# Performance work log

Measured on AMD Instinct MI355X. Metric: run time of the kernel, lower is better.

The kernel has to match this reference:

```python
import jax, jax.numpy as jnp
import numpy as np

B, T, E, H = 1024, 200, 128, 128
N_ITEMS, N_CATS = 100000, 1000
LN_EPS = 1e-5


def _prelu(x, a):
    return jnp.where(x >= 0, x, a * x)


def _layernorm(x, g, b):
    m = x.mean(-1, keepdims=True)
    v = ((x - m) ** 2).mean(-1, keepdims=True)
    return (x - m) / jnp.sqrt(v + LN_EPS) * g + b


def setup_inputs() -> dict:
    key = jax.random.key(0)
    it = iter(jax.random.split(key, 64))
    nx = lambda: next(it)
    def lin(out_d, in_d):
        s = 1.0 / np.sqrt(in_d)
        return jax.random.uniform(nx(), (out_d, in_d), jnp.float32, -s, s)
    inp = {}
    inp['behavior_ids'] = jax.random.randint(nx(), (B, T), 0, N_ITEMS)
    inp['candidate_id'] = jax.random.randint(nx(), (B,), 0, N_ITEMS)
    inp['candidate_cat'] = jax.random.randint(nx(), (B,), 0, N_CATS)
    inp['dense_features'] = jax.random.normal(nx(), (B, 5), jnp.float32)
    inp['item_emb'] = (jax.random.normal(nx(), (N_ITEMS, E), jnp.float32) * 0.01).at[0].set(0.0)
    inp['cat_emb'] = (jax.random.normal(nx(), (N_CATS, E // 2), jnp.float32) * 0.01).at[0].set(0.0)
    # nn.GRU params (gate order r,z,n)
    inp['gru_wih'] = lin(3 * H, E)
    inp['gru_whh'] = lin(3 * H, H)
    inp['gru_bih'] = jnp.zeros((3 * H,), jnp.float32)
    inp['gru_bhh'] = jnp.zeros((3 * H,), jnp.float32)
    # auxiliary_net: Linear(H,E) -> ReLU -> Linear(E,1)
    inp['aux_w1'] = lin(E, H); inp['aux_b1'] = jnp.zeros((E,), jnp.float32)
    inp['aux_w2'] = lin(1, E); inp['aux_b2'] = jnp.zeros((1,), jnp.float32)
    # attention_mlp: Linear(3H,64) -> PReLU -> Linear(64,1)
    inp['att_w1'] = lin(64, 3 * H); inp['att_b1'] = jnp.zeros((64,), jnp.float32)
    inp['att_a'] = jnp.array(0.25, jnp.float32)
    inp['att_w2'] = lin(1, 64); inp['att_b2'] = jnp.zeros((1,), jnp.float32)
    # AUGRU gates: Linear(2H, H) each
    inp['wz'] = lin(H, 2 * H); inp['bz'] = jnp.zeros((H,), jnp.float32)
    inp['wr'] = lin(H, 2 * H); inp['br'] = jnp.zeros((H,), jnp.float32)
    inp['wh'] = lin(H, 2 * H); inp['bh'] = jnp.zeros((H,), jnp.float32)
    # dense_proj Linear(5,32)
    inp['dp_w'] = lin(32, 5); inp['dp_b'] = jnp.zeros((32,), jnp.float32)
    # MLP: 352 -> 256 -> 128 -> 64, each Linear + LayerNorm + PReLU
    dims = [H + E + E // 2 + 32, 256, 128, 64]
    for i in range(3):
        inp[f'm_w{i+1}'] = lin(dims[i + 1], dims[i])
        inp[f'm_b{i+1}'] = jnp.zeros((dims[i + 1],), jnp.float32)
        inp[f'ln_g{i+1}'] = jnp.ones((dims[i + 1],), jnp.float32)
        inp[f'ln_b{i+1}'] = jnp.zeros((dims[i + 1],), jnp.float32)
        inp[f'pa{i+1}'] = jnp.array(0.25, jnp.float32)
    # 3 task heads Linear(64,1), stacked
    inp['heads_w'] = lin(3, 64); inp['heads_b'] = jnp.zeros((3,), jnp.float32)
    return inp


def _forward_core(behavior_ids, candidate_id, candidate_cat, dense_features,
                  item_emb, cat_emb, gru_wih, gru_whh, gru_bih, gru_bhh,
                  aux_w1, aux_b1, aux_w2, aux_b2,
                  att_w1, att_b1, att_a, att_w2, att_b2,
                  wz, bz, wr, br, wh, bh, dp_w, dp_b,
                  m_w1, m_b1, ln_g1, ln_b1, pa1,
                  m_w2, m_b2, ln_g2, ln_b2, pa2,
                  m_w3, m_b3, ln_g3, ln_b3, pa3,
                  heads_w, heads_b):
    beh = item_emb[behavior_ids]            # [B,T,E]
    cand = item_emb[candidate_id]           # [B,E]
    catv = cat_emb[candidate_cat]           # [B,E//2]
    Bsz = beh.shape[0]
    Hd = gru_whh.shape[1]
    h0 = jnp.zeros((Bsz, Hd), beh.dtype)
    # --- interest extractor GRU (cuDNN GRU math, gate order r,z,n) ---
    xp = jnp.einsum('bte,ge->btg', beh, gru_wih) + gru_bih  # [B,T,3H]
    def gru_step(h, x):
        hp = h @ gru_whh.T + gru_bhh
        xr, xz, xn = jnp.split(x, 3, -1)
        hr, hz, hn = jnp.split(hp, 3, -1)
        r = jax.nn.sigmoid(xr + hr)
        z = jax.nn.sigmoid(xz + hz)
        n = jnp.tanh(xn + r * hn)
        hnew = (1 - z) * n + z * h
        return hnew, hnew
    _, hs = jax.lax.scan(gru_step, h0, jnp.swapaxes(xp, 0, 1))
    hs = jnp.swapaxes(hs, 0, 1)             # [B,T,H]
    # --- auxiliary logits ---
    aux = jax.nn.relu(hs[:, :-1] @ aux_w1.T + aux_b1) @ aux_w2.T + aux_b2  # [B,T-1,1]
    # --- attention (embed_dim == hidden_size so cand_proj == candidate_emb) ---
    ce = cand[:, None, :]
    att_in = jnp.concatenate([hs, jnp.broadcast_to(ce, hs.shape), hs * ce], -1)  # [B,T,3H]
    scores = (_prelu(att_in @ att_w1.T + att_b1, att_a) @ att_w2.T + att_b2)[..., 0]
    att = jax.nn.softmax(scores, axis=-1)   # [B,T]
    # --- AUGRU: attention-modulated update gate ---
    def augru_step(h, xs):
        x, a = xs                           # x: [B,H], a: [B]
        comb = jnp.concatenate([x, h], -1)
        z = jax.nn.sigmoid(comb @ wz.T + bz)
        r = jax.nn.sigmoid(comb @ wr.T + br)
        comb_r = jnp.concatenate([x, r * h], -1)
        ht = jnp.tanh(comb_r @ wh.T + bh)
        zp = a[:, None] * z
        return (1 - zp) * h + zp * ht, None
    hT, _ = jax.lax.scan(augru_step, h0, (jnp.swapaxes(hs, 0, 1), att.T))
    # --- fusion MLP (dropout is identity in eval) ---
    dense_out = dense_features @ dp_w.T + dp_b
    x = jnp.concatenate([hT, cand, catv, dense_out], -1)  # [B,352]
    for (w, b, g, be, a) in ((m_w1, m_b1, ln_g1, ln_b1, pa1),
                             (m_w2, m_b2, ln_g2, ln_b2, pa2),
                             (m_w3, m_b3, ln_g3, ln_b3, pa3)):
        x = _prelu(_layernorm(x @ w.T + b, g, be), a)
    preds = jax.nn.sigmoid(x @ heads_w.T + heads_b)  # [B,3] == 3 heads of [B,1]
    return preds, aux


def reference(behavior_ids, candidate_id, candidate_cat, dense_features,
              item_emb, cat_emb, gru_wih, gru_whh, gru_bih, gru_bhh,
              aux_w1, aux_b1, aux_w2, aux_b2,
              att_w1, att_b1, att_a, att_w2, att_b2,
              wz, bz, wr, br, wh, bh, dp_w, dp_b,
              m_w1, m_b1, ln_g1, ln_b1, pa1,
              m_w2, m_b2, ln_g2, ln_b2, pa2,
              m_w3, m_b3, ln_g3, ln_b3, pa3,
              heads_w, heads_b):
    return _forward_core(behavior_ids, candidate_id, candidate_cat, dense_features,
                         item_emb, cat_emb, gru_wih, gru_whh, gru_bih, gru_bhh,
                         aux_w1, aux_b1, aux_w2, aux_b2,
                         att_w1, att_b1, att_a, att_w2, att_b2,
                         wz, bz, wr, br, wh, bh, dp_w, dp_b,
                         m_w1, m_b1, ln_g1, ln_b1, pa1,
                         m_w2, m_b2, ln_g2, ln_b2, pa2,
                         m_w3, m_b3, ln_g3, ln_b3, pa3,
                         heads_w, heads_b)
```

## Files before the change

### kernel.cpp

```cpp
#include <hip/hip_runtime.h>


typedef __bf16 bf16;
typedef float f32x4 __attribute__((ext_vector_type(4)));
typedef __bf16 bf16x8 __attribute__((ext_vector_type(8)));
typedef __bf16 bf16x4 __attribute__((ext_vector_type(4)));

#define MFMA16(a, b, c) __builtin_amdgcn_mfma_f32_16x16x32_bf16((a), (b), (c), 0, 0, 0)

#define BATCH 1024
#define SEQT 200
#define F32_ONE 0x3F800000u

__device__ __forceinline__ float sigm(float x) {
  return __builtin_amdgcn_rcpf(1.0f + __expf(-x));
}
__device__ __forceinline__ float tanh_fast(float x) {
  float ax = fabsf(x);
  float t = 1.0f - 2.0f * __builtin_amdgcn_rcpf(__expf(2.0f * ax) + 1.0f);
  return copysignf(t, x);
}

__device__ __forceinline__ void bar_lgkm() {
  asm volatile("s_waitcnt lgkmcnt(0)\n\ts_barrier" ::: "memory");
// ... 3 lines not shown
  __builtin_amdgcn_global_load_lds((__attribute__((address_space(1))) void*)g,
                                   (__attribute__((address_space(3))) void*)l,
                                   16, 0, 0);
}

template <typename DT> __device__ __forceinline__ float ldf(const DT* p, long i);
template <> __device__ __forceinline__ float ldf<bf16>(const bf16* p, long i) { return (float)p[i]; }
template <> __device__ __forceinline__ float ldf<float>(const float* p, long i) { return p[i]; }

template <typename DT> __device__ __forceinline__ bf16x8 ld8(const DT* p, long i);
template <> __device__ __forceinline__ bf16x8 ld8<bf16>(const bf16* p, long i) {
  return *(const bf16x8*)(p + i);
}
template <> __device__ __forceinline__ bf16x8 ld8<float>(const float* p, long i) {
  f32x4 a = *(const f32x4*)(p + i);
  f32x4 b = *(const f32x4*)(p + i + 4);
  bf16x8 r;
  r[0] = (bf16)a[0]; r[1] = (bf16)a[1]; r[2] = (bf16)a[2]; r[3] = (bf16)a[3];
  r[4] = (bf16)b[0]; r[5] = (bf16)b[1]; r[6] = (bf16)b[2]; r[7] = (bf16)b[3];
  return r;
}

template <typename DT>
__device__ __forceinline__ void prep_body(
    const int* __restrict__ cid, const int* __restrict__ ccat,
    const DT* __restrict__ dense, const DT* __restrict__ item_emb,
    const DT* __restrict__ cat_emb, const DT* __restrict__ dp_w,
    const DT* __restrict__ dp_b, bf16* __restrict__ candbuf, bf16* __restrict__ xf) {
  const int b = blockIdx.x;
  const int t = threadIdx.x;
  bf16 v = (bf16)ldf(item_emb, (long)cid[b] * 128 + t);
  candbuf[b * 128 + t] = v;
  xf[(long)b * 352 + 128 + t] = v;
  if (t < 64) xf[(long)b * 352 + 256 + t] = (bf16)ldf(cat_emb, (long)ccat[b] * 64 + t);
  if (t < 32) {
    float s = ldf(dp_b, t);
    for (int k = 0; k < 5; k++) s += ldf(dense, b * 5 + k) * ldf(dp_w, t * 5 + k);
    xf[(long)b * 352 + 320 + t] = (bf16)s;
  }
}
__global__ __launch_bounds__(128) void k_prep(
    const unsigned* __restrict__ disc, const int* cid, const int* ccat,
    const void* dense, const void* item_emb, const void* cat_emb,
    const void* dp_w, const void* dp_b, bf16* candbuf, bf16* xf) {
  if (*disc == F32_ONE)
    prep_body<float>(cid, ccat, (const float*)dense, (const float*)item_emb,
                     (const float*)cat_emb, (const float*)dp_w, (const float*)dp_b, candbuf, xf);
  else
    prep_body<bf16>(cid, ccat, (const bf16*)dense, (const bf16*)item_emb,
                    (const bf16*)cat_emb, (const bf16*)dp_w, (const bf16*)dp_b, candbuf, xf);
}

template <typename DT>
__device__ __forceinline__ void gru3_body(
    const int* __restrict__ ids, const DT* __restrict__ item_emb,
    const DT* __restrict__ wih, const DT* __restrict__ whh,
    const DT* __restrict__ bih, const DT* __restrict__ bhh, bf16* __restrict__ hs,
    bf16 (*hA)[16][136], bf16 (*xb)[4][16][136], char* raw) {
  const int b0 = blockIdx.x * 16;
  const int tid = threadIdx.x;
  const int w = tid >> 6, lane = tid & 63, l15 = lane & 15, quad = lane >> 4;
  const int nc = w * 16 + l15;

  for (int i = tid; i < 2 * 16 * 136; i += 512) ((bf16*)hA)[i] = (bf16)0.0f;

  bf16x8 wir[4], wiz[4], win_[4], whr[4], whz[4], whn[4];
#pragma unroll
  for (int k = 0; k < 4; k++) {
    const long off = k * 32 + quad * 8;
    wir[k] = ld8(wih, (long)nc * 128 + off);
    wiz[k] = ld8(wih, (long)(128 + nc) * 128 + off);
    win_[k] = ld8(wih, (long)(256 + nc) * 128 + off);
    whr[k] = ld8(whh, (long)nc * 128 + off);
    whz[k] = ld8(whh, (long)(128 + nc) * 128 + off);
    whn[k] = ld8(whh, (long)(256 + nc) * 128 + off);
  }
  const float br_s = ldf(bih, nc) + ldf(bhh, nc);
  const float bz_s = ldf(bih, 128 + nc) + ldf(bhh, 128 + nc);
  const float bxn_s = ldf(bih, 256 + nc);
  const float bhn_s = ldf(bhh, 256 + nc);

  const int idrow = (sizeof(DT) == 4) ? (tid >> 5) : ((tid >> 4) & 15);
  const int* idbase = ids + (long)(b0 + idrow) * SEQT;

  auto DMA = [&](const int4 id4) {
    if constexpr (sizeof(DT) == 4) {
#pragma unroll
      for (int j = 0; j < 4; j++)
        dma16((const char*)(item_emb + (long)((&id4.x)[j]) * 128) + (tid & 31) * 16,
              raw + (j * 512 + tid) * 16);
    } else {
#pragma unroll
      for (int j = 0; j < 2; j++) {
        const int slot = j * 2 + (tid >> 8);
        dma16((const char*)(item_emb + (long)((&id4.x)[slot]) * 128) + (tid & 15) * 16,
              raw + (j * 512 + tid) * 16);
      }
    }
  };
  auto CONV = [&](int buf) {
    if constexpr (sizeof(DT) == 4) {
      const float* rf = (const float*)raw;
#pragma unroll
      for (int h = 0; h < 4; h++) {
        const int e = h * 2048 + tid * 4;
        f32x4 a = *(const f32x4*)(rf + e);
        const int slot = e >> 11, row = (e >> 7) & 15, col = e & 127;
        bf16x4 o;
        o[0] = (bf16)a[0]; o[1] = (bf16)a[1]; o[2] = (bf16)a[2]; o[3] = (bf16)a[3];
        *(bf16x4*)&xb[buf][slot][row][col] = o;
      }
    } else {
      const bf16* rh = (const bf16*)raw;
#pragma unroll
      for (int h = 0; h < 2; h++) {
        const int e = h * 4096 + tid * 8;
        const int slot = e >> 11, row = (e >> 7) & 15, col = e & 127;
        *(bf16x8*)&xb[buf][slot][row][col] = *(const bf16x8*)(rh + e);
      }
    }
  };

  const int srow = tid >> 5, sch = (tid & 31) * 4;
  bf16* hsb = hs + ((long)(b0 + srow) * SEQT) * 128 + sch;

  float hreg[4] = {0.f, 0.f, 0.f, 0.f};
  const f32x4 z4 = {0.f, 0.f, 0.f, 0.f};

  int4 idv = *(const int4*)(idbase);
  DMA(idv);
  idv = *(const int4*)(idbase + 4);
  asm volatile("s_waitcnt vmcnt(1)" ::: "memory");
  __builtin_amdgcn_sched_barrier(0);
  __builtin_amdgcn_s_barrier();
  CONV(0);
  asm volatile("s_waitcnt lgkmcnt(0)" ::: "memory");
  __builtin_amdgcn_sched_barrier(0);
  __builtin_amdgcn_s_barrier();
  DMA(idv);
  idv = *(const int4*)(idbase + 8);

#define GRU_STEP(P, S)                                                         \
  {                                                                            \
    const int tt = t0 + (S);                                                   \
    bf16x8 af[4], xaf[4];                                                      \
    _Pragma("unroll") for (int k = 0; k < 4; k++) {                            \
      af[k] = *(const bf16x8*)&hA[P][l15][k * 32 + quad * 8];                  \
      xaf[k] = *(const bf16x8*)&xb[buf][S][l15][k * 32 + quad * 8];            \
    }                                                                          \
    { const int slot = tt ? tt - 1 : 0;                                        \
      bf16x4 hv = *(const bf16x4*)&hA[P][srow][sch];                           \
      *(bf16x4*)(hsb + (long)slot * 128) = hv; }                               \
    f32x4 ar = z4, az = z4, axn = z4, ahn = z4;                                \
    _Pragma("unroll") for (int k = 0; k < 4; k++) {                            \
      ar = MFMA16(xaf[k], wir[k], ar);                                         \
      az = MFMA16(xaf[k], wiz[k], az);                                         \
      axn = MFMA16(xaf[k], win_[k], axn);                                      \
    }                                                                          \
    _Pragma("unroll") for (int k = 0; k < 4; k++) {                            \
      ar = MFMA16(af[k], whr[k], ar);                                          \
      az = MFMA16(af[k], whz[k], az);                                          \
      ahn = MFMA16(af[k], whn[k], ahn);                                        \
    }                                                                          \
    _Pragma("unroll") for (int r = 0; r < 4; r++) {                            \
      float r_ = sigm(ar[r] + br_s);                                           \
      float z_ = sigm(az[r] + bz_s);                                           \
      float n_ = tanh_fast(axn[r] + bxn_s + r_ * (ahn[r] + bhn_s));            \
      float hnew = (1.0f - z_) * n_ + z_ * hreg[r];                            \
      hreg[r] = hnew;                                                          \
      hA[(P) ^ 1][quad * 4 + r][nc] = (bf16)hnew;                              \
    }                                                                          \
    bar_lgkm();                                                                \
  }

  for (int c = 0; c < 50; c++) {
    const int t0 = c * 4;
    const int buf = c & 1;
    GRU_STEP(0, 0) GRU_STEP(1, 1) GRU_STEP(0, 2) GRU_STEP(1, 3)
    if (c < 49) {
      asm volatile("s_waitcnt vmcnt(4)" ::: "memory");
      __builtin_amdgcn_sched_barrier(0);
      __builtin_amdgcn_s_barrier();
      CONV((c + 1) & 1);
      asm volatile("s_waitcnt lgkmcnt(0)" ::: "memory");
      __builtin_amdgcn_sched_barrier(0);
      __builtin_amdgcn_s_barrier();
      if (c < 48) {
        DMA(idv);
        int nid = (c + 3) * 4; if (nid > 196) nid = 196;
        idv = *(const int4*)(idbase + nid);
      }
    }
  }
#undef GRU_STEP
  { bf16x4 hv = *(const bf16x4*)&hA[0][srow][sch];
    *(bf16x4*)(hsb + (long)(SEQT - 1) * 128) = hv; }
}
__global__ __launch_bounds__(512, 1) void k_gru3(
    const unsigned* __restrict__ disc, const int* ids, const void* item_emb,
    const void* wih, const void* whh, const void* bih, const void* bhh, bf16* hs) {
  __shared__ __align__(16) bf16 hA[2][16][136];
  __shared__ __align__(16) bf16 xb[2][4][16][136];
  __shared__ __align__(16) char raw[32768];
  if (*disc == F32_ONE)
    gru3_body<float>(ids, (const float*)item_emb, (const float*)wih, (const float*)whh,
                     (const float*)bih, (const float*)bhh, hs, hA, xb, raw);
  else
    gru3_body<bf16>(ids, (const bf16*)item_emb, (const bf16*)wih, (const bf16*)whh,
                    (const bf16*)bih, (const bf16*)bhh, hs, hA, xb, raw);
}

template <typename DT>
__device__ __forceinline__ void attaux_body(
    const bf16* __restrict__ hs, const int* __restrict__ cid,
    const DT* __restrict__ item_emb,
    const DT* __restrict__ aw1, const DT* __restrict__ ab1,
    const DT* __restrict__ aw2, const DT* __restrict__ ab2,
    const DT* __restrict__ tw1, const DT* __restrict__ tb1, const DT* __restrict__ ta,
    const DT* __restrict__ tw2, const DT* __restrict__ tb2,
    float* __restrict__ sc, float* __restrict__ outaux,
    bf16 (*As)[64][128], float (*scPt)[64], float (*scPa)[64]) {
  const int t0 = blockIdx.x * 64;
  const int b0 = blockIdx.y * 16;
  const int tid = threadIdx.x, w = tid >> 6, lane = tid & 63, l15 = lane & 15, quad = lane >> 4;

  const int tn = w * 16 + l15;
  bf16x8 wth[4], wtc[4], wthc[4], wa0[4], wa1[4];
#pragma unroll
  for (int k = 0; k < 4; k++) {
    const long off = k * 32 + quad * 8;
    wth[k]  = ld8(tw1, (long)tn * 384 + off);
    wtc[k]  = ld8(tw1, (long)tn * 384 + 128 + off);
    wthc[k] = ld8(tw1, (long)tn * 384 + 256 + off);
    wa0[k]  = ld8(aw1, (long)((2 * w) * 16 + l15) * 128 + off);
    wa1[k]  = ld8(aw1, (long)((2 * w + 1) * 16 + l15) * 128 + off);
  }
  const float tb1c = ldf(tb1, tn), tw2c = ldf(tw2, tn);
  const float ab1c0 = ldf(ab1, (2 * w) * 16 + l15), aw2c0 = ldf(aw2, (2 * w) * 16 + l15);
  const float ab1c1 = ldf(ab1, (2 * w + 1) * 16 + l15), aw2c1 = ldf(aw2, (2 * w + 1) * 16 + l15);
  const float aP = ldf(ta, 0), tb2s = ldf(tb2, 0), ab2s = ldf(ab2, 0);

  auto DMA = [&](int b, int buf) {
#pragma unroll
    for (int c = 0; c < 4; c++) {
      const int idx = c * 256 + tid;
      const int row = idx >> 4, p = idx & 15;
      int t = t0 + row; if (t > SEQT - 1) t = SEQT - 1;
      const bf16* src = hs + ((long)b * SEQT + t) * 128 + ((p ^ (row & 7)) * 8);
      dma16(src, (char*)(&As[buf][0][0]) + idx * 16);
    }
  };
  auto CANDLD = [&](int b, bf16x8* cf) {
#pragma unroll
    for (int k = 0; k < 4; k++)
      cf[k] = ld8(item_emb, (long)cid[b] * 128 + k * 32 + quad * 8);
  };

  const f32x4 z4 = {0.f, 0.f, 0.f, 0.f};
  bf16x8 candA[4], candB[4];
  DMA(b0, 0);
  CANDLD(b0, candA);
  asm volatile("s_waitcnt vmcnt(0)" ::: "memory");
// ... 54 lines not shown
      int tt2 = tid - 64, t = t0 + tt2;                                        \
      if (t < SEQT - 1) {                                                      \
        float s = scPa[0][tt2] + scPa[1][tt2] + scPa[2][tt2] + scPa[3][tt2];   \
        outaux[(long)b * 199 + t] = s + ab2s;                                  \
      }                                                                        \
    }                                                                          \
    asm volatile("s_waitcnt vmcnt(0) lgkmcnt(0)" ::: "memory");                \
    __builtin_amdgcn_sched_barrier(0);                                         \
    __builtin_amdgcn_s_barrier();                                              \
  }

  for (int bi = 0; bi < 16; bi += 2) {
    AA_STEP(bi, candA, candB)
    AA_STEP(bi + 1, candB, candA)
  }
#undef AA_STEP
}
__global__ __launch_bounds__(256, 1) void k_attaux(
    const unsigned* __restrict__ disc, const bf16* hs, const int* cid,
    const void* item_emb,
    const void* aw1, const void* ab1, const void* aw2, const void* ab2,
    const void* tw1, const void* tb1, const void* ta, const void* tw2, const void* tb2,
    float* sc, float* outaux) {
  __shared__ __align__(16) bf16 As[2][64][128];
  __shared__ __align__(16) float scPt[4][64];
  __shared__ __align__(16) float scPa[4][64];
  if (*disc == F32_ONE)
    attaux_body<float>(hs, cid, (const float*)item_emb,
                       (const float*)aw1, (const float*)ab1, (const float*)aw2, (const float*)ab2,
                       (const float*)tw1, (const float*)tb1, (const float*)ta,
                       (const float*)tw2, (const float*)tb2, sc, outaux, As, scPt, scPa);
  else
    attaux_body<bf16>(hs, cid, (const bf16*)item_emb,
                      (const bf16*)aw1, (const bf16*)ab1, (const bf16*)aw2, (const bf16*)ab2,
                      (const bf16*)tw1, (const bf16*)tb1, (const bf16*)ta,
                      (const bf16*)tw2, (const bf16*)tb2, sc, outaux, As, scPt, scPa);
}

__global__ __launch_bounds__(256) void k_softmax(float* __restrict__ sc) {
  const int b = blockIdx.x, tid = threadIdx.x;
  __shared__ float red[256];
  float v = (tid < SEQT) ? sc[(long)b * SEQT + tid] : -1e30f;
  red[tid] = v; __syncthreads();
  for (int s = 128; s > 0; s >>= 1) { if (tid < s) red[tid] = fmaxf(red[tid], red[tid + s]); __syncthreads(); }
  float mx = red[0]; __syncthreads();
  float e = (tid < SEQT) ? __expf(v - mx) : 0.f;
  red[tid] = e; __syncthreads();
  for (int s = 128; s > 0; s >>= 1) { if (tid < s) red[tid] += red[tid + s]; __syncthreads(); }
  float inv = 1.0f / red[0];
  if (tid < SEQT) sc[(long)b * SEQT + tid] = e * inv;
}

template <typename DT>
__device__ __forceinline__ void augru3_body(
    const bf16* __restrict__ hsrc, const float* __restrict__ att,
    const DT* __restrict__ wz, const DT* __restrict__ wr, const DT* __restrict__ wh,
    const DT* __restrict__ bzv, const DT* __restrict__ brv, const DT* __restrict__ bhv,
    bf16* __restrict__ xf_out,
    bf16 (*hA)[16][136], bf16 (*rhA)[136], float (*attL)[201],
    bf16 (*xb)[4][16][136], char* raw) {
  const int b0 = blockIdx.x * 16;
  const int tid = threadIdx.x;
  const int w = tid >> 6, lane = tid & 63, l15 = lane & 15, quad = lane >> 4;
  const int nc = w * 16 + l15;

  for (int i = tid; i < 2 * 16 * 136; i += 512) ((bf16*)hA)[i] = (bf16)0.0f;
  for (int i = tid; i < 16 * SEQT; i += 512) {
    int r = i / SEQT, c = i - r * SEQT;
    attL[r][c] = att[(long)(b0 + r) * SEQT + c];
  }

  bf16x8 wzx[4], wzh[4], wrx[4], wrh[4], whx[4], whh_[4];
#pragma unroll
  for (int k = 0; k < 4; k++) {
    const long off = k * 32 + quad * 8;
    wzx[k] = ld8(wz, (long)nc * 256 + off);
    wzh[k] = ld8(wz, (long)nc * 256 + 128 + off);
    wrx[k] = ld8(wr, (long)nc * 256 + off);
    wrh[k] = ld8(wr, (long)nc * 256 + 128 + off);
    whx[k] = ld8(wh, (long)nc * 256 + off);
    whh_[k] = ld8(wh, (long)nc * 256 + 128 + off);
  }
  const float bz_s = ldf(bzv, nc);
  const float br_s = ldf(brv, nc);
  const float bh_s = ldf(bhv, nc);

  auto DMA = [&](int t0) {
#pragma unroll
    for (int j = 0; j < 2; j++) {
      const int slot = j * 2 + (tid >> 8);
      const int row = (tid >> 4) & 15;
      const bf16* src = hsrc + ((long)(b0 + row) * SEQT + t0 + slot) * 128 + (tid & 15) * 8;
      dma16(src, raw + (j * 512 + tid) * 16);
    }
  };
  auto CONV = [&](int buf) {
    const bf16* rh = (const bf16*)raw;
#pragma unroll
    for (int h = 0; h < 2; h++) {
      const int e = h * 4096 + tid * 8;
      const int slot = e >> 11, row = (e >> 7) & 15, col = e & 127;
      *(bf16x8*)&xb[buf][slot][row][col] = *(const bf16x8*)(rh + e);
    }
  };

  float hreg[4] = {0.f, 0.f, 0.f, 0.f};
  const f32x4 z4 = {0.f, 0.f, 0.f, 0.f};

  DMA(0);
  asm volatile("s_waitcnt vmcnt(0)" ::: "memory");
  __builtin_amdgcn_sched_barrier(0);
  __builtin_amdgcn_s_barrier();
  CONV(0);
  asm volatile("s_waitcnt lgkmcnt(0)" ::: "memory");
  __builtin_amdgcn_sched_barrier(0);
  __builtin_amdgcn_s_barrier();
  DMA(4);

#define AUGRU_STEP(P, S)                                                       \
  {                                                                            \
    const int tt = t0 + (S);                                                   \
    bf16x8 af[4], xaf[4];                                                      \
    _Pragma("unroll") for (int k = 0; k < 4; k++) {                            \
      af[k] = *(const bf16x8*)&hA[P][l15][k * 32 + quad * 8];                  \
      xaf[k] = *(const bf16x8*)&xb[buf][S][l15][k * 32 + quad * 8];            \
    }                                                                          \
    f32x4 az = z4, ar = z4, axh = z4;                                          \
    _Pragma("unroll") for (int k = 0; k < 4; k++) {                            \
      az = MFMA16(xaf[k], wzx[k], az);                                         \
      ar = MFMA16(xaf[k], wrx[k], ar);                                         \
      axh = MFMA16(xaf[k], whx[k], axh);                                       \
    }                                                                          \
    _Pragma("unroll") for (int k = 0; k < 4; k++) {                            \
      az = MFMA16(af[k], wzh[k], az);                                          \
      ar = MFMA16(af[k], wrh[k], ar);                                          \
    }                                                                          \
    float zp[4];                                                               \
    _Pragma("unroll") for (int r = 0; r < 4; r++) {                            \
      float a_ = attL[quad * 4 + r][tt];                                       \
      float z_ = sigm(az[r] + bz_s);                                           \
      float r_ = sigm(ar[r] + br_s);                                           \
      zp[r] = a_ * z_;                                                         \
      rhA[quad * 4 + r][nc] = (bf16)(r_ * hreg[r]);                            \
    }                                                                          \
    bar_lgkm();                                                                \
    bf16x8 rf[4];                                                              \
    _Pragma("unroll") for (int k = 0; k < 4; k++)                              \
      rf[k] = *(const bf16x8*)&rhA[l15][k * 32 + quad * 8];                    \
    f32x4 ahh = axh;                                                           \
    _Pragma("unroll") for (int k = 0; k < 4; k++)                              \
      ahh = MFMA16(rf[k], whh_[k], ahh);                                       \
    _Pragma("unroll") for (int r = 0; r < 4; r++) {                            \
      float ht = tanh_fast(ahh[r] + bh_s);                                     \
      float hnew = (1.f - zp[r]) * hreg[r] + zp[r] * ht;                       \
      hreg[r] = hnew;                                                          \
      hA[(P) ^ 1][quad * 4 + r][nc] = (bf16)hnew;                              \
    }                                                                          \
    bar_lgkm();                                                                \
  }

  for (int c = 0; c < 50; c++) {
    const int t0 = c * 4;
    const int buf = c & 1;
    AUGRU_STEP(0, 0) AUGRU_STEP(1, 1) AUGRU_STEP(0, 2) AUGRU_STEP(1, 3)
    if (c < 49) {
      asm volatile("s_waitcnt vmcnt(0)" ::: "memory");
      __builtin_amdgcn_sched_barrier(0);
      __builtin_amdgcn_s_barrier();
      CONV((c + 1) & 1);
      asm volatile("s_waitcnt lgkmcnt(0)" ::: "memory");
      __builtin_amdgcn_sched_barrier(0);
      __builtin_amdgcn_s_barrier();
      if (c < 48) DMA((c + 2) * 4);
    }
  }
#undef AUGRU_STEP
#pragma unroll
  for (int r = 0; r < 4; r++)
    xf_out[(long)(b0 + quad * 4 + r) * 352 + nc] = (bf16)hreg[r];
}
__global__ __launch_bounds__(512, 1) void k_augru3(
    const unsigned* __restrict__ disc, const bf16* hsrc, const float* att,
    const void* wz, const void* wr, const void* wh,
    const void* bzv, const void* brv, const void* bhv, bf16* xf_out) {
  __shared__ __align__(16) bf16 hA[2][16][136];
  __shared__ __align__(16) bf16 rhA[16][136];
  __shared__ __align__(16) float attL[16][201];
  __shared__ __align__(16) bf16 xb[2][4][16][136];
  __shared__ __align__(16) char raw[16384];
  if (*disc == F32_ONE)
    augru3_body<float>(hsrc, att, (const float*)wz, (const float*)wr, (const float*)wh,
                       (const float*)bzv, (const float*)brv, (const float*)bhv, xf_out,
                       hA, rhA, attL, xb, raw);
  else
    augru3_body<bf16>(hsrc, att, (const bf16*)wz, (const bf16*)wr, (const bf16*)wh,
                      (const bf16*)bzv, (const bf16*)brv, (const bf16*)bhv, xf_out,
                      hA, rhA, attL, xb, raw);
}

template <typename DT>
__device__ __forceinline__ void mlp_body(
    const bf16* __restrict__ xf,
    const DT* __restrict__ w1, const DT* __restrict__ b1, const DT* __restrict__ g1, const DT* __restrict__ be1, const DT* __restrict__ pa1,
    const DT* __restrict__ w2, const DT* __restrict__ b2, const DT* __restrict__ g2, const DT* __restrict__ be2, const DT* __restrict__ pa2,
    const DT* __restrict__ w3, const DT* __restrict__ b3, const DT* __restrict__ g3, const DT* __restrict__ be3, const DT* __restrict__ pa3,
    const DT* __restrict__ hw, const DT* __restrict__ hb, float* __restrict__ preds,
    float (*xs)[352], float (*ys)[256]) {
  const int tid = threadIdx.x, w = tid >> 6, lane = tid & 63;
  const int b = blockIdx.x * 4 + w;
  for (int i = lane; i < 352; i += 64) xs[w][i] = (float)xf[(long)b * 352 + i];
  __syncthreads();
  float acc1[4];
#pragma unroll
  for (int oi = 0; oi < 4; oi++) {
    int o = lane + 64 * oi;
    float s = ldf(b1, o);
    for (int k = 0; k < 352; k += 8) {
      bf16x8 wv = ld8(w1, (long)o * 352 + k);
#pragma unroll
      for (int j = 0; j < 8; j++) s += xs[w][k + j] * (float)wv[j];
    }
    acc1[oi] = s;
  }
  float sm = acc1[0] + acc1[1] + acc1[2] + acc1[3];
#pragma unroll
  for (int m = 1; m < 64; m <<= 1) sm += __shfl_xor(sm, m, 64);
  float mean = sm * (1.0f / 256.0f);
  float vs = 0.f;
#pragma unroll
  for (int oi = 0; oi < 4; oi++) { float d = acc1[oi] - mean; vs += d * d; }
#pragma unroll
  for (int m = 1; m < 64; m <<= 1) vs += __shfl_xor(vs, m, 64);
  float rstd = rsqrtf(vs * (1.0f / 256.0f) + 1e-5f);
  float a1 = ldf(pa1, 0);
#pragma unroll
  for (int oi = 0; oi < 4; oi++) {
    int o = lane + 64 * oi;
    float y = (acc1[oi] - mean) * rstd * ldf(g1, o) + ldf(be1, o);
    ys[w][o] = (y >= 0.f) ? y : a1 * y;
  }
  __syncthreads();
  float acc2[2];
#pragma unroll
  for (int oi = 0; oi < 2; oi++) {
    int o = lane + 64 * oi;
    float s = ldf(b2, o);
    for (int k = 0; k < 256; k += 8) {
      bf16x8 wv = ld8(w2, (long)o * 256 + k);
#pragma unroll
      for (int j = 0; j < 8; j++) s += ys[w][k + j] * (float)wv[j];
// ... 77 lines not shown
  const void* item_emb = d_in[4];
  const void* cat_emb = d_in[5];
  const void* gru_wih = d_in[6];
  const void* gru_whh = d_in[7];
  const void* gru_bih = d_in[8];
  const void* gru_bhh = d_in[9];
  const void* aux_w1 = d_in[10];
  const void* aux_b1 = d_in[11];
  const void* aux_w2 = d_in[12];
  const void* aux_b2 = d_in[13];
  const void* att_w1 = d_in[14];
  const void* att_b1 = d_in[15];
  const void* att_a = d_in[16];
  const void* att_w2 = d_in[17];
  const void* att_b2 = d_in[18];
  const void* wz = d_in[19];
  const void* bz = d_in[20];
  const void* wr = d_in[21];
  const void* br = d_in[22];
  const void* wh = d_in[23];
  const void* bh = d_in[24];
  const void* dp_w = d_in[25];
  const void* dp_b = d_in[26];
  const void* m_w1 = d_in[27];
  const void* m_b1 = d_in[28];
  const void* ln_g1 = d_in[29];
  const void* ln_b1 = d_in[30];
  const void* pa1 = d_in[31];
  const void* m_w2 = d_in[32];
  const void* m_b2 = d_in[33];
  const void* ln_g2 = d_in[34];
  const void* ln_b2 = d_in[35];
  const void* pa2 = d_in[36];
  const void* m_w3 = d_in[37];
  const void* m_b3 = d_in[38];
  const void* ln_g3 = d_in[39];
  const void* ln_b3 = d_in[40];
  const void* pa3 = d_in[41];
  const void* heads_w = d_in[42];
  const void* heads_b = d_in[43];
  (void)in_sizes; (void)n_in; (void)out_size; (void)ws_size;

  const unsigned* disc = (const unsigned*)ln_g1;

  char* ws = (char*)d_ws;
  bf16* HS = (bf16*)(ws);
  float* SC = (float*)(ws + 52428800L);
  bf16* CAND = (bf16*)(ws + 53248000L);
  bf16* XF = (bf16*)(ws + 53510144L);
  float* OUT = (float*)d_out;

  k_prep<<<BATCH, 128, 0, stream>>>(disc, candidate_id, candidate_cat, dense, item_emb,
                                    cat_emb, dp_w, dp_b, CAND, XF);
  k_gru3<<<64, 512, 0, stream>>>(disc, behavior_ids, item_emb, gru_wih, gru_whh,
                                 gru_bih, gru_bhh, HS);
  k_attaux<<<dim3(4, 64), 256, 0, stream>>>(disc, HS, candidate_id, item_emb,
                                            aux_w1, aux_b1, aux_w2, aux_b2,
                                            att_w1, att_b1, att_a, att_w2, att_b2,
                                            SC, OUT + 3072);
  k_softmax<<<BATCH, 256, 0, stream>>>(SC);
  k_augru3<<<64, 512, 0, stream>>>(disc, HS, SC, wz, wr, wh, bz, br, bh, XF);
  k_mlp<<<256, 256, 0, stream>>>(disc, XF,
      m_w1, m_b1, ln_g1, ln_b1, pa1,
      m_w2, m_b2, ln_g2, ln_b2, pa2,
      m_w3, m_b3, ln_g3, ln_b3, pa3,
      heads_w, heads_b, OUT);
}
```

Before: 727.2 us.

## Process two independent 16-row batch groups per block in GRU and AUGRU kernels

Each GRU and AUGRU block now carries two independent 16-sequence groups through the recurrence, interleaving their MFMA chains and sharing the register-resident weight fragments, so the grid drops from 64 to 32 blocks. The aim is to hide MFMA and transcendental latency on the serial recurrence by giving each wave two independent dependency chains per barrier. The cost is half as many blocks on a GPU with many CUs, plus higher register and LDS use that could cause spills.

```diff
diff --git a/kernel.cpp b/kernel.cpp
--- a/kernel.cpp
+++ b/kernel.cpp
@@ -79,17 +79,17 @@
 }
 
 template <typename DT>
-__device__ __forceinline__ void gru3_body(
+__device__ __forceinline__ void gru4_body(
     const int* __restrict__ ids, const DT* __restrict__ item_emb,
     const DT* __restrict__ wih, const DT* __restrict__ whh,
     const DT* __restrict__ bih, const DT* __restrict__ bhh, bf16* __restrict__ hs,
-    bf16 (*hA)[16][136], bf16 (*xb)[4][16][136], char* raw) {
-  const int b0 = blockIdx.x * 16;
+    bf16 (*hA)[2][16][136], bf16 (*xb)[2][4][16][136], char* raw) {
+  const int b0 = blockIdx.x * 32;
   const int tid = threadIdx.x;
   const int w = tid >> 6, lane = tid & 63, l15 = lane & 15, quad = lane >> 4;
   const int nc = w * 16 + l15;
 
-  for (int i = tid; i < 2 * 16 * 136; i += 512) ((bf16*)hA)[i] = (bf16)0.0f;
+  for (int i = tid; i < 2 * 2 * 16 * 136; i += 512) ((bf16*)hA)[i] = (bf16)0.0f;
 
   bf16x8 wir[4], wiz[4], win_[4], whr[4], whz[4], whn[4];
 #pragma unroll
@@ -108,94 +108,121 @@
   const float bhn_s = ldf(bhh, 256 + nc);
 
   const int idrow = (sizeof(DT) == 4) ? (tid >> 5) : ((tid >> 4) & 15);
-  const int* idbase = ids + (long)(b0 + idrow) * SEQT;
-
-  auto DMA = [&](const int4 id4) {
+  const int* idbaseA = ids + (long)(b0 + idrow) * SEQT;
+  const int* idbaseB = ids + (long)(b0 + 16 + idrow) * SEQT;
+
+  auto DMA = [&](int p, const int4 id4) {
+    char* rp = raw + p * 32768;
     if constexpr (sizeof(DT) == 4) {
 #pragma unroll
       for (int j = 0; j < 4; j++)
         dma16((const char*)(item_emb + (long)((&id4.x)[j]) * 128) + (tid & 31) * 16,
-              raw + (j * 512 + tid) * 16);
+              rp + (j * 512 + tid) * 16);
     } else {
 #pragma unroll
       for (int j = 0; j < 2; j++) {
         const int slot = j * 2 + (tid >> 8);
         dma16((const char*)(item_emb + (long)((&id4.x)[slot]) * 128) + (tid & 15) * 16,
-              raw + (j * 512 + tid) * 16);
+              rp + (j * 512 + tid) * 16);
       }
     }
   };
   auto CONV = [&](int buf) {
-    if constexpr (sizeof(DT) == 4) {
-      const float* rf = (const float*)raw;
-#pragma unroll
-      for (int h = 0; h < 4; h++) {
-        const int e = h * 2048 + tid * 4;
-        f32x4 a = *(const f32x4*)(rf + e);
-        const int slot = e >> 11, row = (e >> 7) & 15, col = e & 127;
-        bf16x4 o;
-        o[0] = (bf16)a[0]; o[1] = (bf16)a[1]; o[2] = (bf16)a[2]; o[3] = (bf16)a[3];
-        *(bf16x4*)&xb[buf][slot][row][col] = o;
+#pragma unroll
+    for (int p = 0; p < 2; p++) {
+      if constexpr (sizeof(DT) == 4) {
+        const float* rf = (const float*)(raw + p * 32768);
+#pragma unroll
+        for (int h = 0; h < 4; h++) {
+          const int e = h * 2048 + tid * 4;
+          f32x4 a = *(const f32x4*)(rf + e);
+          const int slot = e >> 11, row = (e >> 7) & 15, col = e & 127;
+          bf16x4 o;
+          o[0] = (bf16)a[0]; o[1] = (bf16)a[1]; o[2] = (bf16)a[2]; o[3] = (bf16)a[3];
+          *(bf16x4*)&xb[p][buf][slot][row][col] = o;
+        }
+      } else {
+        const bf16* rh = (const bf16*)(raw + p * 32768);
+#pragma unroll
+        for (int h = 0; h < 2; h++) {
+          const int e = h * 4096 + tid * 8;
+          const int slot = e >> 11, row = (e >> 7) & 15, col = e & 127;
+          *(bf16x8*)&xb[p][buf][slot][row][col] = *(const bf16x8*)(rh + e);
+        }
       }
-    } else {
-      const bf16* rh = (const bf16*)raw;
-#pragma unroll
-      for (int h = 0; h < 2; h++) {
-        const int e = h * 4096 + tid * 8;
-        const int slot = e >> 11, row = (e >> 7) & 15, col = e & 127;
-        *(bf16x8*)&xb[buf][slot][row][col] = *(const bf16x8*)(rh + e);
-      }
     }
   };
 
   const int srow = tid >> 5, sch = (tid & 31) * 4;
-  bf16* hsb = hs + ((long)(b0 + srow) * SEQT) * 128 + sch;
-
-  float hreg[4] = {0.f, 0.f, 0.f, 0.f};
+  bf16* hsbA = hs + ((long)(b0 + srow) * SEQT) * 128 + sch;
+  bf16* hsbB = hs + ((long)(b0 + 16 + srow) * SEQT) * 128 + sch;
+
+  float hregA[4] = {0.f, 0.f, 0.f, 0.f};
+  float hregB[4] = {0.f, 0.f, 0.f, 0.f};
   const f32x4 z4 = {0.f, 0.f, 0.f, 0.f};
 
-  int4 idv = *(const int4*)(idbase);
-  DMA(idv);
-  idv = *(const int4*)(idbase + 4);
-  asm volatile("s_waitcnt vmcnt(1)" ::: "memory");
+  int4 idvA = *(const int4*)(idbaseA);
+  int4 idvB = *(const int4*)(idbaseB);
+  DMA(0, idvA); DMA(1, idvB);
+  idvA = *(const int4*)(idbaseA + 4);
+  idvB = *(const int4*)(idbaseB + 4);
+  asm volatile("s_waitcnt vmcnt(2)" ::: "memory");
   __builtin_amdgcn_sched_barrier(0);
   __builtin_amdgcn_s_barrier();
   CONV(0);
   asm volatile("s_waitcnt lgkmcnt(0)" ::: "memory");
   __builtin_amdgcn_sched_barrier(0);
   __builtin_amdgcn_s_barrier();
-  DMA(idv);
-  idv = *(const int4*)(idbase + 8);
-
-#define GRU_STEP(P, S)                                                         \
+  DMA(0, idvA); DMA(1, idvB);
+  idvA = *(const int4*)(idbaseA + 8);
+  idvB = *(const int4*)(idbaseB + 8);
+
+#define GRU_STEP2(P, S)                                                        \
   {                                                                            \
     const int tt = t0 + (S);                                                   \
-    bf16x8 af[4], xaf[4];                                                      \
+    bf16x8 afA[4], xafA[4], afB[4], xafB[4];                                   \
     _Pragma("unroll") for (int k = 0; k < 4; k++) {                            \
-      af[k] = *(const bf16x8*)&hA[P][l15][k * 32 + quad * 8];                  \
-      xaf[k] = *(const bf16x8*)&xb[buf][S][l15][k * 32 + quad * 8];            \
+      afA[k] = *(const bf16x8*)&hA[0][P][l15][k * 32 + quad * 8];              \
+      xafA[k] = *(const bf16x8*)&xb[0][buf][S][l15][k * 32 + quad * 8];        \
+      afB[k] = *(const bf16x8*)&hA[1][P][l15][k * 32 + quad * 8];              \
+      xafB[k] = *(const bf16x8*)&xb[1][buf][S][l15][k * 32 + quad * 8];        \
     }                                                                          \
     { const int slot = tt ? tt - 1 : 0;                                        \
-      bf16x4 hv = *(const bf16x4*)&hA[P][srow][sch];                           \
-      *(bf16x4*)(hsb + (long)slot * 128) = hv; }                               \
-    f32x4 ar = z4, az = z4, axn = z4, ahn = z4;                                \
+      bf16x4 hvA = *(const bf16x4*)&hA[0][P][srow][sch];                       \
+      bf16x4 hvB = *(const bf16x4*)&hA[1][P][srow][sch];                       \
+      *(bf16x4*)(hsbA + (long)slot * 128) = hvA;                               \
+      *(bf16x4*)(hsbB + (long)slot * 128) = hvB; }                             \
+    f32x4 arA = z4, azA = z4, axnA = z4, ahnA = z4;                            \
+    f32x4 arB = z4, azB = z4, axnB = z4, ahnB = z4;                            \
     _Pragma("unroll") for (int k = 0; k < 4; k++) {                            \
-      ar = MFMA16(xaf[k], wir[k], ar);                                         \
-      az = MFMA16(xaf[k], wiz[k], az);                                         \
-      axn = MFMA16(xaf[k], win_[k], axn);                                      \
+      arA = MFMA16(xafA[k], wir[k], arA);                                      \
+      azA = MFMA16(xafA[k], wiz[k], azA);                                      \
+      axnA = MFMA16(xafA[k], win_[k], axnA);                                   \
+      arB = MFMA16(xafB[k], wir[k], arB);                                      \
+      azB = MFMA16(xafB[k], wiz[k], azB);                                      \
+      axnB = MFMA16(xafB[k], win_[k], axnB);                                   \
     }                                                                          \
     _Pragma("unroll") for (int k = 0; k < 4; k++) {                            \
-      ar = MFMA16(af[k], whr[k], ar);                                          \
-      az = MFMA16(af[k], whz[k], az);                                          \
-      ahn = MFMA16(af[k], whn[k], ahn);                                        \
+      arA = MFMA16(afA[k], whr[k], arA);                                       \
+      azA = MFMA16(afA[k], whz[k], azA);                                       \
+      ahnA = MFMA16(afA[k], whn[k], ahnA);                                     \
+      arB = MFMA16(afB[k], whr[k], arB);                                       \
+      azB = MFMA16(afB[k], whz[k], azB);                                       \
+      ahnB = MFMA16(afB[k], whn[k], ahnB);                                     \
     }                                                                          \
     _Pragma("unroll") for (int r = 0; r < 4; r++) {                            \
-      float r_ = sigm(ar[r] + br_s);                                           \
-      float z_ = sigm(az[r] + bz_s);                                           \
-      float n_ = tanh_fast(axn[r] + bxn_s + r_ * (ahn[r] + bhn_s));            \
-      float hnew = (1.0f - z_) * n_ + z_ * hreg[r];                            \
-      hreg[r] = hnew;                                                          \
-      hA[(P) ^ 1][quad * 4 + r][nc] = (bf16)hnew;                              \
+      float rA_ = sigm(arA[r] + br_s);                                         \
+      float zA_ = sigm(azA[r] + bz_s);                                         \
+      float nA_ = tanh_fast(axnA[r] + bxn_s + rA_ * (ahnA[r] + bhn_s));        \
+      float hnA = (1.0f - zA_) * nA_ + zA_ * hregA[r];                         \
+      hregA[r] = hnA;                                                          \
+      hA[0][(P) ^ 1][quad * 4 + r][nc] = (bf16)hnA;                            \
+      float rB_ = sigm(arB[r] + br_s);                                         \
+      float zB_ = sigm(azB[r] + bz_s);                                         \
+      float nB_ = tanh_fast(axnB[r] + bxn_s + rB_ * (ahnB[r] + bhn_s));        \
+      float hnB = (1.0f - zB_) * nB_ + zB_ * hregB[r];                         \
+      hregB[r] = hnB;                                                          \
+      hA[1][(P) ^ 1][quad * 4 + r][nc] = (bf16)hnB;                            \
     }                                                                          \
     bar_lgkm();                                                                \
   }
@@ -203,9 +230,9 @@
   for (int c = 0; c < 50; c++) {
     const int t0 = c * 4;
     const int buf = c & 1;
-    GRU_STEP(0, 0) GRU_STEP(1, 1) GRU_STEP(0, 2) GRU_STEP(1, 3)
+    GRU_STEP2(0, 0) GRU_STEP2(1, 1) GRU_STEP2(0, 2) GRU_STEP2(1, 3)
     if (c < 49) {
-      asm volatile("s_waitcnt vmcnt(4)" ::: "memory");
+      asm volatile("s_waitcnt vmcnt(10)" ::: "memory");
       __builtin_amdgcn_sched_barrier(0);
       __builtin_amdgcn_s_barrier();
       CONV((c + 1) & 1);
@@ -213,28 +240,31 @@
       __builtin_amdgcn_sched_barrier(0);
       __builtin_amdgcn_s_barrier();
       if (c < 48) {
-        DMA(idv);
+        DMA(0, idvA); DMA(1, idvB);
         int nid = (c + 3) * 4; if (nid > 196) nid = 196;
-        idv = *(const int4*)(idbase + nid);
+        idvA = *(const int4*)(idbaseA + nid);
+        idvB = *(const int4*)(idbaseB + nid);
       }
     }
   }
-#undef GRU_STEP
-  { bf16x4 hv = *(const bf16x4*)&hA[0][srow][sch];
-    *(bf16x4*)(hsb + (long)(SEQT - 1) * 128) = hv; }
-}
-__global__ __launch_bounds__(512, 1) void k_gru3(
+#undef GRU_STEP2
+  { bf16x4 hvA = *(const bf16x4*)&hA[0][0][srow][sch];
+    bf16x4 hvB = *(const bf16x4*)&hA[1][0][srow][sch];
+    *(bf16x4*)(hsbA + (long)(SEQT - 1) * 128) = hvA;
+    *(bf16x4*)(hsbB + (long)(SEQT - 1) * 128) = hvB; }
+}
+__global__ __launch_bounds__(512, 1) void k_gru4(
     const unsigned* __restrict__ disc, const int* ids, const void* item_emb,
     const void* wih, const void* whh, const void* bih, const void* bhh, bf16* hs) {
-  __shared__ __align__(16) bf16 hA[2][16][136];
-  __shared__ __align__(16) bf16 xb[2][4][16][136];
-  __shared__ __align__(16) char raw[32768];
+  __shared__ __align__(16) bf16 hA[2][2][16][136];
+  __shared__ __align__(16) bf16 xb[2][2][4][16][136];
+  __shared__ __align__(16) char raw[2][32768];
   if (*disc == F32_ONE)
-    gru3_body<float>(ids, (const float*)item_emb, (const float*)wih, (const float*)whh,
-                     (const float*)bih, (const float*)bhh, hs, hA, xb, raw);
+    gru4_body<float>(ids, (const float*)item_emb, (const float*)wih, (const float*)whh,
+                     (const float*)bih, (const float*)bhh, hs, hA, xb, (char*)raw);
   else
-    gru3_body<bf16>(ids, (const bf16*)item_emb, (const bf16*)wih, (const bf16*)whh,
-                    (const bf16*)bih, (const bf16*)bhh, hs, hA, xb, raw);
+    gru4_body<bf16>(ids, (const bf16*)item_emb, (const bf16*)wih, (const bf16*)whh,
+                    (const bf16*)bih, (const bf16*)bhh, hs, hA, xb, (char*)raw);
 }
 
 template <typename DT>
@@ -395,22 +425,24 @@
 }
 
 template <typename DT>
-__device__ __forceinline__ void augru3_body(
+__device__ __forceinline__ void augru4_body(
     const bf16* __restrict__ hsrc, const float* __restrict__ att,
     const DT* __restrict__ wz, const DT* __restrict__ wr, const DT* __restrict__ wh,
     const DT* __restrict__ bzv, const DT* __restrict__ brv, const DT* __restrict__ bhv,
     bf16* __restrict__ xf_out,
-    bf16 (*hA)[16][136], bf16 (*rhA)[136], float (*attL)[201],
-    bf16 (*xb)[4][16][136], char* raw) {
-  const int b0 = blockIdx.x * 16;
+    bf16 (*hA)[2][16][136], bf16 (*rhA)[16][136], float (*attL)[16][201],
+    bf16 (*xb)[2][4][16][136], char* raw) {
+  const int b0 = blockIdx.x * 32;
   const int tid = threadIdx.x;
   const int w = tid >> 6, lane = tid & 63, l15 = lane & 15, quad = lane >> 4;
   const int nc = w * 16 + l15;
 
-  for (int i = tid; i < 2 * 16 * 136; i += 512) ((bf16*)hA)[i] = (bf16)0.0f;
-  for (int i = tid; i < 16 * SEQT; i += 512) {
-    int r = i / SEQT, c = i - r * SEQT;
-    attL[r][c] = att[(long)(b0 + r) * SEQT + c];
+  for (int i = tid; i < 2 * 2 * 16 * 136; i += 512) ((bf16*)hA)[i] = (bf16)0.0f;
+  for (int i = tid; i < 2 * 16 * SEQT; i += 512) {
+    int p = i / (16 * SEQT);
+    int rem = i - p * 16 * SEQT;
+    int r = rem / SEQT, c = rem - r * SEQT;
+    attL[p][r][c] = att[(long)(b0 + p * 16 + r) * SEQT + c];
   }
 
   bf16x8 wzx[4], wzh[4], wrx[4], wrh[4], whx[4], whh_[4];
@@ -428,29 +460,35 @@
   const float br_s = ldf(brv, nc);
   const float bh_s = ldf(bhv, nc);
 
-  auto DMA = [&](int t0) {
+  auto DMA = [&](int p, int t0) {
+    char* rp = raw + p * 16384;
 #pragma unroll
     for (int j = 0; j < 2; j++) {
       const int slot = j * 2 + (tid >> 8);
       const int row = (tid >> 4) & 15;
-      const bf16* src = hsrc + ((long)(b0 + row) * SEQT + t0 + slot) * 128 + (tid & 15) * 8;
-      dma16(src, raw + (j * 512 + tid) * 16);
+      const bf16* src =
+          hsrc + ((long)(b0 + p * 16 + row) * SEQT + t0 + slot) * 128 + (tid & 15) * 8;
+      dma16(src, rp + (j * 512 + tid) * 16);
     }
   };
   auto CONV = [&](int buf) {
-    const bf16* rh = (const bf16*)raw;
-#pragma unroll
-    for (int h = 0; h < 2; h++) {
-      const int e = h * 4096 + tid * 8;
-      const int slot = e >> 11, row = (e >> 7) & 15, col = e & 127;
-      *(bf16x8*)&xb[buf][slot][row][col] = *(const bf16x8*)(rh + e);
+#pragma unroll
+    for (int p = 0; p < 2; p++) {
+      const bf16* rh = (const bf16*)(raw + p * 16384);
+#pragma unroll
+      for (int h = 0; h < 2; h++) {
+        const int e = h * 4096 + tid * 8;
+        const int slot = e >> 11, row = (e >> 7) & 15, col = e & 127;
+        *(bf16x8*)&xb[p][buf][slot][row][col] = *(const bf16x8*)(rh + e);
+      }
     }
   };
 
-  float hreg[4] = {0.f, 0.f, 0.f, 0.f};
+  float hregA[4] = {0.f, 0.f, 0.f, 0.f};
+  float hregB[4] = {0.f, 0.f, 0.f, 0.f};
   const f32x4 z4 = {0.f, 0.f, 0.f, 0.f};
 
-  DMA(0);
+  DMA(0, 0); DMA(1, 0);
   asm volatile("s_waitcnt vmcnt(0)" ::: "memory");
   __builtin_amdgcn_sched_barrier(0);
   __builtin_amdgcn_s_barrier();
@@ -458,46 +496,67 @@
   asm volatile("s_waitcnt lgkmcnt(0)" ::: "memory");
   __builtin_amdgcn_sched_barrier(0);
   __builtin_amdgcn_s_barrier();
-  DMA(4);
-
-#define AUGRU_STEP(P, S)                                                       \
+  DMA(0, 4); DMA(1, 4);
+
+#define AUGRU_STEP2(P, S)                                                      \
   {                                                                            \
     const int tt = t0 + (S);                                                   \
-    bf16x8 af[4], xaf[4];                                                      \
+    bf16x8 afA[4], xafA[4], afB[4], xafB[4];                                   \
     _Pragma("unroll") for (int k = 0; k < 4; k++) {                            \
-      af[k] = *(const bf16x8*)&hA[P][l15][k * 32 + quad * 8];                  \
-      xaf[k] = *(const bf16x8*)&xb[buf][S][l15][k * 32 + quad * 8];            \
-    }                                                                          \
-    f32x4 az = z4, ar = z4, axh = z4;                                          \
+      afA[k] = *(const bf16x8*)&hA[0][P][l15][k * 32 + quad * 8];              \
+      xafA[k] = *(const bf16x8*)&xb[0][buf][S][l15][k * 32 + quad * 8];        \
+      afB[k] = *(const bf16x8*)&hA[1][P][l15][k * 32 + quad * 8];              \
+      xafB[k] = *(const bf16x8*)&xb[1][buf][S][l15][k * 32 + quad * 8];        \
+    }                                                                          \
+    f32x4 azA = z4, arA = z4, axhA = z4;                                       \
+    f32x4 azB = z4, arB = z4, axhB = z4;                                       \
     _Pragma("unroll") for (int k = 0; k < 4; k++) {                            \
-      az = MFMA16(xaf[k], wzx[k], az);                                         \
-      ar = MFMA16(xaf[k], wrx[k], ar);                                         \
-      axh = MFMA16(xaf[k], whx[k], axh);                                       \
+      azA = MFMA16(xafA[k], wzx[k], azA);                                      \
+      arA = MFMA16(xafA[k], wrx[k], arA);                                      \
+      axhA = MFMA16(xafA[k], whx[k], axhA);                                    \
+      azB = MFMA16(xafB[k], wzx[k], azB);                                      \
+      arB = MFMA16(xafB[k], wrx[k], arB);                                      \
+      axhB = MFMA16(xafB[k], whx[k], axhB);                                    \
     }                                                                          \
     _Pragma("unroll") for (int k = 0; k < 4; k++) {                            \
-      az = MFMA16(af[k], wzh[k], az);                                          \
-      ar = MFMA16(af[k], wrh[k], ar);                                          \
-    }                                                                          \
-    float zp[4];                                                               \
+      azA = MFMA16(afA[k], wzh[k], azA);                                       \
+      arA = MFMA16(afA[k], wrh[k], arA);                                       \
+      azB = MFMA16(afB[k], wzh[k], azB);                                       \
+      arB = MFMA16(afB[k], wrh[k], arB);                                       \
+    }                                                                          \
+    float zpA[4], zpB[4];                                                      \
     _Pragma("unroll") for (int r = 0; r < 4; r++) {                            \
-      float a_ = attL[quad * 4 + r][tt];                                       \
-      float z_ = sigm(az[r] + bz_s);                                           \
-      float r_ = sigm(ar[r] + br_s);                                           \
-      zp[r] = a_ * z_;                                                         \
-      rhA[quad * 4 + r][nc] = (bf16)(r_ * hreg[r]);                            \
+      float aA_ = attL[0][quad * 4 + r][tt];                                   \
+      float zA_ = sigm(azA[r] + bz_s);                                         \
+      float rA_ = sigm(arA[r] + br_s);                                         \
+      zpA[r] = aA_ * zA_;                                                      \
+      rhA[0][quad * 4 + r][nc] = (bf16)(rA_ * hregA[r]);                       \
+      float aB_ = attL[1][quad * 4 + r][tt];                                   \
+      float zB_ = sigm(azB[r] + bz_s);                                         \
+      float rB_ = sigm(arB[r] + br_s);                                         \
+      zpB[r] = aB_ * zB_;                                                      \
+      rhA[1][quad * 4 + r][nc] = (bf16)(rB_ * hregB[r]);                       \
     }                                                                          \
     bar_lgkm();                                                                \
-    bf16x8 rf[4];                                                              \
-    _Pragma("unroll") for (int k = 0; k < 4; k++)                              \
-      rf[k] = *(const bf16x8*)&rhA[l15][k * 32 + quad * 8];                    \
-    f32x4 ahh = axh;                                                           \
-    _Pragma("unroll") for (int k = 0; k < 4; k++)                              \
-      ahh = MFMA16(rf[k], whh_[k], ahh);                                       \
+    bf16x8 rfA[4], rfB[4];                                                     \
+    _Pragma("unroll") for (int k = 0; k < 4; k++) {                            \
+      rfA[k] = *(const bf16x8*)&rhA[0][l15][k * 32 + quad * 8];                \
+      rfB[k] = *(const bf16x8*)&rhA[1][l15][k * 32 + quad * 8];                \
+    }                                                                          \
+    f32x4 ahhA = axhA, ahhB = axhB;                                            \
+    _Pragma("unroll") for (int k = 0; k < 4; k++) {                            \
+      ahhA = MFMA16(rfA[k], whh_[k], ahhA);                                    \
+      ahhB = MFMA16(rfB[k], whh_[k], ahhB);                                    \
+    }                                                                          \
     _Pragma("unroll") for (int r = 0; r < 4; r++) {                            \
-      float ht = tanh_fast(ahh[r] + bh_s);                                     \
-      float hnew = (1.f - zp[r]) * hreg[r] + zp[r] * ht;                       \
-      hreg[r] = hnew;                                                          \
-      hA[(P) ^ 1][quad * 4 + r][nc] = (bf16)hnew;                              \
+      float htA = tanh_fast(ahhA[r] + bh_s);                                   \
+      float hnA = (1.f - zpA[r]) * hregA[r] + zpA[r] * htA;                    \
+      hregA[r] = hnA;                                                          \
+      hA[0][(P) ^ 1][quad * 4 + r][nc] = (bf16)hnA;                            \
+      float htB = tanh_fast(ahhB[r] + bh_s);                                   \
+      float hnB = (1.f - zpB[r]) * hregB[r] + zpB[r] * htB;                    \
+      hregB[r] = hnB;                                                          \
+      hA[1][(P) ^ 1][quad * 4 + r][nc] = (bf16)hnB;                            \
     }                                                                          \
     bar_lgkm();                                                                \
   }
@@ -505,7 +564,7 @@
   for (int c = 0; c < 50; c++) {
     const int t0 = c * 4;
     const int buf = c & 1;
-    AUGRU_STEP(0, 0) AUGRU_STEP(1, 1) AUGRU_STEP(0, 2) AUGRU_STEP(1, 3)
+    AUGRU_STEP2(0, 0) AUGRU_STEP2(1, 1) AUGRU_STEP2(0, 2) AUGRU_STEP2(1, 3)
     if (c < 49) {
       asm volatile("s_waitcnt vmcnt(0)" ::: "memory");
       __builtin_amdgcn_sched_barrier(0);
@@ -514,31 +573,33 @@
       asm volatile("s_waitcnt lgkmcnt(0)" ::: "memory");
       __builtin_amdgcn_sched_barrier(0);
       __builtin_amdgcn_s_barrier();
-      if (c < 48) DMA((c + 2) * 4);
-    }
-  }
-#undef AUGRU_STEP
-#pragma unroll
-  for (int r = 0; r < 4; r++)
-    xf_out[(long)(b0 + quad * 4 + r) * 352 + nc] = (bf16)hreg[r];
-}
-__global__ __launch_bounds__(512, 1) void k_augru3(
+      if (c < 48) { DMA(0, (c + 2) * 4); DMA(1, (c + 2) * 4); }
+    }
+  }
+#undef AUGRU_STEP2
+#pragma unroll
+  for (int r = 0; r < 4; r++) {
+    xf_out[(long)(b0 + quad * 4 + r) * 352 + nc] = (bf16)hregA[r];
+    xf_out[(long)(b0 + 16 + quad * 4 + r) * 352 + nc] = (bf16)hregB[r];
+  }
+}
+__global__ __launch_bounds__(512, 1) void k_augru4(
     const unsigned* __restrict__ disc, const bf16* hsrc, const float* att,
     const void* wz, const void* wr, const void* wh,
     const void* bzv, const void* brv, const void* bhv, bf16* xf_out) {
-  __shared__ __align__(16) bf16 hA[2][16][136];
-  __shared__ __align__(16) bf16 rhA[16][136];
-  __shared__ __align__(16) float attL[16][201];
-  __shared__ __align__(16) bf16 xb[2][4][16][136];
-  __shared__ __align__(16) char raw[16384];
+  __shared__ __align__(16) bf16 hA[2][2][16][136];
+  __shared__ __align__(16) bf16 rhA[2][16][136];
+  __shared__ __align__(16) float attL[2][16][201];
+  __shared__ __align__(16) bf16 xb[2][2][4][16][136];
+  __shared__ __align__(16) char raw[2][16384];
   if (*disc == F32_ONE)
-    augru3_body<float>(hsrc, att, (const float*)wz, (const float*)wr, (const float*)wh,
+    augru4_body<float>(hsrc, att, (const float*)wz, (const float*)wr, (const float*)wh,
                        (const float*)bzv, (const float*)brv, (const float*)bhv, xf_out,
-                       hA, rhA, attL, xb, raw);
+                       hA, rhA, attL, xb, (char*)raw);
   else
-    augru3_body<bf16>(hsrc, att, (const bf16*)wz, (const bf16*)wr, (const bf16*)wh,
+    augru4_body<bf16>(hsrc, att, (const bf16*)wz, (const bf16*)wr, (const bf16*)wh,
                       (const bf16*)bzv, (const bf16*)brv, (const bf16*)bhv, xf_out,
-                      hA, rhA, attL, xb, raw);
+                      hA, rhA, attL, xb, (char*)raw);
 }
 
 template <typename DT>
@@ -722,14 +783,14 @@
 
   k_prep<<<BATCH, 128, 0, stream>>>(disc, candidate_id, candidate_cat, dense, item_emb,
                                     cat_emb, dp_w, dp_b, CAND, XF);
-  k_gru3<<<64, 512, 0, stream>>>(disc, behavior_ids, item_emb, gru_wih, gru_whh,
+  k_gru4<<<32, 512, 0, stream>>>(disc, behavior_ids, item_emb, gru_wih, gru_whh,
                                  gru_bih, gru_bhh, HS);
   k_attaux<<<dim3(4, 64), 256, 0, stream>>>(disc, HS, candidate_id, item_emb,
                                             aux_w1, aux_b1, aux_w2, aux_b2,
                                             att_w1, att_b1, att_a, att_w2, att_b2,
                                             SC, OUT + 3072);
   k_softmax<<<BATCH, 256, 0, stream>>>(SC);
-  k_augru3<<<64, 512, 0, stream>>>(disc, HS, SC, wz, wr, wh, bz, br, bh, XF);
+  k_augru4<<<32, 512, 0, stream>>>(disc, HS, SC, wz, wr, wh, bz, br, bh, XF);
   k_mlp<<<256, 256, 0, stream>>>(disc, XF,
       m_w1, m_b1, ln_g1, ln_b1, pa1,
       m_w2, m_b2, ln_g2, ln_b2, pa2,
```

Measured after the change: 1.073 ms. 1.48x slower.
